# Optimization experiments

Hardware: AMD Instinct MI355X
Metric: run time of the kernel (lower is better)

Reference implementation:

```python
import jax, jax.numpy as jnp
import numpy as np

N, K, D = 50000, 32, 128


def setup_inputs() -> dict:
    key = jax.random.key(0)
    k1, k2, k3, k4 = jax.random.split(key, 4)
    v_fea = jax.random.normal(k1, (N, D), dtype=jnp.float32)
    t_emb = jax.random.normal(k2, (N, D), dtype=jnp.float32)
    ef = jax.random.randint(k3, (N, K), 0, N, dtype=jnp.int64)
    # nn.Linear(2D, 2D, bias=False) weight, scaled like torch default init
    W = jax.random.normal(k4, (2 * D, 2 * D), dtype=jnp.float32) * (1.0 / np.sqrt(2 * D))
    return {"v_fea": v_fea, "t_emb": t_emb, "ef": ef, "W": W}


def reference(v_fea, t_emb, ef, W):
    # v: gathered neighbor features [N, K, D]
    v = v_fea[ef]
    # q: [N, 2D]; torch Linear applies x @ W.T
    q = jnp.concatenate([v_fea, t_emb], axis=-1)
    wq = q @ W.T                                   # [N, 2D]
    # k: [N, K, 2D]
    k = jnp.concatenate([v, t_emb[ef]], axis=-1)
    # per-edge score: bmm(k, wq[..., None]) -> [N, K]
    r = jnp.einsum("nkd,nd->nk", k, wq)
    r = jax.nn.softmax(r, axis=1)                  # softmax over neighbors
    # weighted sum over neighbors -> [N, D]
    ef_fea = jnp.einsum("nk,nkd->nd", r, v)
    return ef_fea
```

## Files before the change

kernel.cpp:

```cpp
#include <hip/hip_runtime.h>
#include <hip/hip_bf16.h>

#define D     128
#define TWO_D 256
#define KNB   32

typedef __attribute__((ext_vector_type(8))) short    s8;
typedef __attribute__((ext_vector_type(8))) _Float16 h8;
typedef __attribute__((ext_vector_type(2))) _Float16 h2v;
typedef __attribute__((ext_vector_type(4))) float    f4;

__device__ inline unsigned short f2h(float f) {
    return __builtin_bit_cast(unsigned short, (_Float16)f);
}
__device__ inline float h2f(unsigned int u) {
    return (float)__builtin_bit_cast(_Float16, (unsigned short)u);
}

union v16u { s8 s; h2v h[4]; };

__device__ inline float dot8(s8 x, s8 w, float acc) {
#if __has_builtin(__builtin_amdgcn_fdot2)
    v16u ux, uw; ux.s = x; uw.s = w;
#pragma unroll
    for (int j = 0; j < 4; ++j)
        acc = __builtin_amdgcn_fdot2(ux.h[j], uw.h[j], acc, false);
#else
#pragma unroll
    for (int j = 0; j < 8; ++j)
        acc = fmaf(h2f((unsigned short)x[j]), h2f((unsigned short)w[j]), acc);
#endif
    return acc;
}

__device__ __forceinline__ void gload16(const void* g, void* l) {
    __builtin_amdgcn_global_load_lds(
        (__attribute__((address_space(1))) void*)g,
        (__attribute__((address_space(3))) void*)l, 16, 0, 0);
}

__global__ __launch_bounds__(256) void cast_kernel(
    const float* __restrict__ a, const float* __restrict__ b,
    unsigned short* __restrict__ oa, unsigned short* __restrict__ ob, int n4)
{
    int i = blockIdx.x * 256 + threadIdx.x;
    if (i >= n4) return;
    float4 x = ((const float4*)a)[i];
    float4 y = ((const float4*)b)[i];
    ushort4 px = make_ushort4(f2h(x.x), f2h(x.y), f2h(x.z), f2h(x.w));
    ushort4 py = make_ushort4(f2h(y.x), f2h(y.y), f2h(y.z), f2h(y.w));
    ((ushort4*)oa)[i] = px;
    ((ushort4*)ob)[i] = py;
}

#define BM 128
#define BN 64
#define BK 64
#define LDT 72

__global__ __launch_bounds__(256) void gemm_wq_mfma(
    const unsigned short* __restrict__ vh, const unsigned short* __restrict__ th,
    const float* __restrict__ W, unsigned short* __restrict__ wq_h, int M)
{
    __shared__ unsigned short As[BM][LDT];
    __shared__ unsigned short Bs[BN][LDT];

    const int tid  = threadIdx.x;
    const int w    = tid >> 6;
    const int lane = tid & 63;
    const int quad = lane >> 4;
    const int l16  = lane & 15;
    const int row0 = blockIdx.x * BM;
    const int i0   = blockIdx.y * BN;

    f4 acc[2][4] = {};

    const int arow = tid >> 1;
    const int acol = (tid & 1) * 32;
    int ga = row0 + arow; if (ga >= M) ga = M - 1;
    const int brow = tid >> 2;
    const int bcol = (tid & 3) * 16;

    for (int kt = 0; kt < TWO_D; kt += BK) {
        const unsigned short* srcA = (kt < D) ? vh : th;
        const int kb = kt & (D - 1);
        const unsigned short* pa = srcA + (size_t)ga * D + kb + acol;
        s8 a0 = *(const s8*)(pa);
        s8 a1 = *(const s8*)(pa + 8);
        s8 a2 = *(const s8*)(pa + 16);
        s8 a3 = *(const s8*)(pa + 24);
        const float* pb = W + (size_t)(i0 + brow) * TWO_D + kt + bcol;
        float4 b0 = *(const float4*)(pb);
        float4 b1 = *(const float4*)(pb + 4);
        float4 b2 = *(const float4*)(pb + 8);
        float4 b3 = *(const float4*)(pb + 12);

        __syncthreads();
        *(s8*)&As[arow][acol]      = a0;
        *(s8*)&As[arow][acol + 8]  = a1;
        *(s8*)&As[arow][acol + 16] = a2;
        *(s8*)&As[arow][acol + 24] = a3;
        {
            s8 q0, q1;
            q0[0]=(short)f2h(b0.x); q0[1]=(short)f2h(b0.y); q0[2]=(short)f2h(b0.z); q0[3]=(short)f2h(b0.w);
            q0[4]=(short)f2h(b1.x); q0[5]=(short)f2h(b1.y); q0[6]=(short)f2h(b1.z); q0[7]=(short)f2h(b1.w);
            q1[0]=(short)f2h(b2.x); q1[1]=(short)f2h(b2.y); q1[2]=(short)f2h(b2.z); q1[3]=(short)f2h(b2.w);
            q1[4]=(short)f2h(b3.x); q1[5]=(short)f2h(b3.y); q1[6]=(short)f2h(b3.z); q1[7]=(short)f2h(b3.w);
            *(s8*)&Bs[brow][bcol]     = q0;
            *(s8*)&Bs[brow][bcol + 8] = q1;
        }
        __syncthreads();

#pragma unroll
        for (int s = 0; s < 2; ++s) {
            s8 af0 = *(const s8*)&As[w * 32 + l16][s * 32 + quad * 8];
            s8 af1 = *(const s8*)&As[w * 32 + 16 + l16][s * 32 + quad * 8];
#pragma unroll
            for (int nt = 0; nt < 4; ++nt) {
                s8 bf = *(const s8*)&Bs[nt * 16 + l16][s * 32 + quad * 8];
                acc[0][nt] = __builtin_amdgcn_mfma_f32_16x16x32_f16(
                    __builtin_bit_cast(h8, af0), __builtin_bit_cast(h8, bf), acc[0][nt], 0, 0, 0);
                acc[1][nt] = __builtin_amdgcn_mfma_f32_16x16x32_f16(
                    __builtin_bit_cast(h8, af1), __builtin_bit_cast(h8, bf), acc[1][nt], 0, 0, 0);
            }
        }
    }

#pragma unroll
    for (int mt = 0; mt < 2; ++mt) {
#pragma unroll
        for (int nt = 0; nt < 4; ++nt) {
#pragma unroll
            for (int r = 0; r < 4; ++r) {
                int grow = row0 + w * 32 + mt * 16 + quad * 4 + r;
                if (grow < M)
                    wq_h[(size_t)grow * TWO_D + i0 + nt * 16 + l16] = f2h(acc[mt][nt][r]);
            }
        }
    }
}

__global__ __launch_bounds__(128) void attn_kernel(
    const unsigned short* __restrict__ vh, const unsigned short* __restrict__ th,
    const int* __restrict__ ef, const unsigned short* __restrict__ wq_h,
    float* __restrict__ outp, int M)
{
    __shared__ char L[2][17408];

    const int lane = threadIdx.x & 63;
    const int w    = threadIdx.x >> 6;
    const int n    = blockIdx.x * 2 + w;
    if (n >= M) return;

    char* Lw = &L[w][0];
    const int l16  = lane & 15;
    const int gsel = (lane >> 4) & 1;
    const unsigned short* gsrc = (lane < 32) ? vh : th;

    int eidx = 0;
    if (lane < KNB) eidx = ef[n * KNB + lane];

    gload16(wq_h + (size_t)n * TWO_D + lane * 8, Lw + 16384);
#pragma unroll
    for (int kk = 0; kk < 16; ++kk) {
        int e = __shfl(eidx, 2 * kk + gsel, 64);
        gload16(gsrc + (size_t)e * D + l16 * 8, Lw + kk * 1024);
    }
    __syncthreads();

    const int k     = lane & 31;
    const int tsel  = lane >> 5;
    const int dbase = (k >> 1) * 1024 + (k & 1) * 256 + tsel * 512;
    const int cbase = 16384 + tsel * 256;
    float p = 0.f;
#pragma unroll
    for (int j = 0; j < 16; ++j) {
        int jl = ((j + lane) & 15) * 16;
        s8 x = *(const s8*)(Lw + dbase + jl);
        s8 c = *(const s8*)(Lw + cbase + jl);
        p = dot8(x, c, p);
    }
    p += __shfl_xor(p, 32, 64);

    float mx = p;
#pragma unroll
    for (int off = 16; off > 0; off >>= 1) mx = fmaxf(mx, __shfl_xor(mx, off, 64));
    float ex  = __expf(p - mx);
    float sum = ex;
#pragma unroll
    for (int off = 16; off > 0; off >>= 1) sum += __shfl_xor(sum, off, 64);
    float r = ex / sum;

    float o4[4] = {0.f, 0.f, 0.f, 0.f};
    const int g   = lane >> 5;
    const int dby = (lane & 31) * 8;
#pragma unroll
    for (int kk = 0; kk < 16; ++kk) {
        float rk = __shfl(r, 2 * kk + g, 64);
        uint2 pq = *(const uint2*)(Lw + kk * 1024 + g * 256 + dby);
        o4[0] = fmaf(rk, h2f(pq.x & 0xFFFFu), o4[0]);
        o4[1] = fmaf(rk, h2f(pq.x >> 16),     o4[1]);
        o4[2] = fmaf(rk, h2f(pq.y & 0xFFFFu), o4[2]);
        o4[3] = fmaf(rk, h2f(pq.y >> 16),     o4[3]);
    }
#pragma unroll
    for (int j = 0; j < 4; ++j) o4[j] += __shfl_xor(o4[j], 32, 64);

    if (lane < 32)
        *(float4*)(outp + (size_t)n * D + (lane & 31) * 4) =
            make_float4(o4[0], o4[1], o4[2], o4[3]);
}

extern "C" void kernel_launch(void* const* d_in, const int* in_sizes, int n_in,
                              void* d_out, int out_size, void* d_ws, size_t ws_size,
                              hipStream_t stream)
{
    const float* v_fea = (const float*)d_in[0];
    const float* t_emb = (const float*)d_in[1];
    const int*   ef    = (const int*)d_in[2];
    const float* W     = (const float*)d_in[3];
    float* outp = (float*)d_out;

    const int M = in_sizes[0] / D;
    char* ws = (char*)d_ws;
    unsigned short* wq_h = (unsigned short*)ws;
    unsigned short* vh   = (unsigned short*)(ws + (size_t)M * TWO_D * 2);
    unsigned short* th   = (unsigned short*)(ws + (size_t)M * TWO_D * 2 + (size_t)M * D * 2);

    const int n4 = M * D / 4;
    cast_kernel<<<(n4 + 255) / 256, 256, 0, stream>>>(v_fea, t_emb, vh, th, n4);

    dim3 gg((M + BM - 1) / BM, TWO_D / BN);
    gemm_wq_mfma<<<gg, 256, 0, stream>>>(vh, th, W, wq_h, M);
    attn_kernel<<<M / 2, 128, 0, stream>>>(vh, th, ef, wq_h, outp, M);
}
```

Baseline: 238.6 us.

## Pre-cast W to fp16, single-shot swizzled GEMM tile, split attention rows across two waves

Result: slower. 243.6 us (+2.1%).

```diff
diff --git a/kernel.cpp b/kernel.cpp
--- a/kernel.cpp
+++ b/kernel.cpp
@@ -41,118 +41,100 @@
 
 __global__ __launch_bounds__(256) void cast_kernel(
     const float* __restrict__ a, const float* __restrict__ b,
-    unsigned short* __restrict__ oa, unsigned short* __restrict__ ob, int n4)
-{
-    int i = blockIdx.x * 256 + threadIdx.x;
-    if (i >= n4) return;
-    float4 x = ((const float4*)a)[i];
-    float4 y = ((const float4*)b)[i];
-    ushort4 px = make_ushort4(f2h(x.x), f2h(x.y), f2h(x.z), f2h(x.w));
-    ushort4 py = make_ushort4(f2h(y.x), f2h(y.y), f2h(y.z), f2h(y.w));
-    ((ushort4*)oa)[i] = px;
-    ((ushort4*)ob)[i] = py;
-}
-
-#define BM 128
-#define BN 64
-#define BK 64
-#define LDT 72
+    const float* __restrict__ Wsrc,
+    unsigned short* __restrict__ oa, unsigned short* __restrict__ ob,
+    unsigned short* __restrict__ oW, int n4, int nblkAB, int n4w)
+{
+    int bid = blockIdx.x;
+    if (bid < nblkAB) {
+        int i = bid * 256 + threadIdx.x;
+        if (i >= n4) return;
+        float4 x = ((const float4*)a)[i];
+        float4 y = ((const float4*)b)[i];
+        ((ushort4*)oa)[i] = make_ushort4(f2h(x.x), f2h(x.y), f2h(x.z), f2h(x.w));
+        ((ushort4*)ob)[i] = make_ushort4(f2h(y.x), f2h(y.y), f2h(y.z), f2h(y.w));
+    } else {
+        int i = (bid - nblkAB) * 256 + threadIdx.x;
+        if (i >= n4w) return;
+        float4 x = ((const float4*)Wsrc)[i];
+        ((ushort4*)oW)[i] = make_ushort4(f2h(x.x), f2h(x.y), f2h(x.z), f2h(x.w));
+    }
+}
 
 __global__ __launch_bounds__(256) void gemm_wq_mfma(
     const unsigned short* __restrict__ vh, const unsigned short* __restrict__ th,
-    const float* __restrict__ W, unsigned short* __restrict__ wq_h, int M)
-{
-    __shared__ unsigned short As[BM][LDT];
-    __shared__ unsigned short Bs[BN][LDT];
+    const unsigned short* __restrict__ Wh, unsigned short* __restrict__ wq_h, int M)
+{
+    __shared__ unsigned short Atile[64 * 256];
+    __shared__ unsigned short Btile[64 * 256];
 
     const int tid  = threadIdx.x;
-    const int w    = tid >> 6;
+    const int ww   = tid >> 6;
     const int lane = tid & 63;
     const int quad = lane >> 4;
     const int l16  = lane & 15;
-    const int row0 = blockIdx.x * BM;
-    const int i0   = blockIdx.y * BN;
-
-    f4 acc[2][4] = {};
-
-    const int arow = tid >> 1;
-    const int acol = (tid & 1) * 32;
-    int ga = row0 + arow; if (ga >= M) ga = M - 1;
-    const int brow = tid >> 2;
-    const int bcol = (tid & 3) * 16;
-
-    for (int kt = 0; kt < TWO_D; kt += BK) {
-        const unsigned short* srcA = (kt < D) ? vh : th;
-        const int kb = kt & (D - 1);
-        const unsigned short* pa = srcA + (size_t)ga * D + kb + acol;
-        s8 a0 = *(const s8*)(pa);
-        s8 a1 = *(const s8*)(pa + 8);
-        s8 a2 = *(const s8*)(pa + 16);
-        s8 a3 = *(const s8*)(pa + 24);
-        const float* pb = W + (size_t)(i0 + brow) * TWO_D + kt + bcol;
-        float4 b0 = *(const float4*)(pb);
-        float4 b1 = *(const float4*)(pb + 4);
-        float4 b2 = *(const float4*)(pb + 8);
-        float4 b3 = *(const float4*)(pb + 12);
-
-        __syncthreads();
-        *(s8*)&As[arow][acol]      = a0;
-        *(s8*)&As[arow][acol + 8]  = a1;
-        *(s8*)&As[arow][acol + 16] = a2;
-        *(s8*)&As[arow][acol + 24] = a3;
-        {
-            s8 q0, q1;
-            q0[0]=(short)f2h(b0.x); q0[1]=(short)f2h(b0.y); q0[2]=(short)f2h(b0.z); q0[3]=(short)f2h(b0.w);
-            q0[4]=(short)f2h(b1.x); q0[5]=(short)f2h(b1.y); q0[6]=(short)f2h(b1.z); q0[7]=(short)f2h(b1.w);
-            q1[0]=(short)f2h(b2.x); q1[1]=(short)f2h(b2.y); q1[2]=(short)f2h(b2.z); q1[3]=(short)f2h(b2.w);
-            q1[4]=(short)f2h(b3.x); q1[5]=(short)f2h(b3.y); q1[6]=(short)f2h(b3.z); q1[7]=(short)f2h(b3.w);
-            *(s8*)&Bs[brow][bcol]     = q0;
-            *(s8*)&Bs[brow][bcol + 8] = q1;
+    const int row0 = blockIdx.x * 64;
+    const int i0   = blockIdx.y * 64;
+
+    const int sr = tid >> 2, ss = tid & 3;
+    int ga = row0 + sr; if (ga >= M) ga = M - 1;
+    const unsigned short* asrc = ((ss < 2) ? vh : th) + (size_t)ga * D + (ss & 1) * 64;
+    const unsigned short* bsrc = Wh + (size_t)(i0 + sr) * TWO_D + ss * 64;
+
+    s8 av[8], bv[8];
+#pragma unroll
+    for (int m = 0; m < 8; ++m) av[m] = *(const s8*)(asrc + m * 8);
+#pragma unroll
+    for (int m = 0; m < 8; ++m) bv[m] = *(const s8*)(bsrc + m * 8);
+#pragma unroll
+    for (int m = 0; m < 8; ++m) {
+        int kblk = ss * 8 + m;
+        *(s8*)&Atile[sr * 256 + ((kblk ^ (sr & 7)) * 8)] = av[m];
+        *(s8*)&Btile[sr * 256 + ((kblk ^ (sr & 7)) * 8)] = bv[m];
+    }
+    __syncthreads();
+
+    f4 acc[4] = {};
+    const int ar = ww * 16 + l16;
+#pragma unroll
+    for (int s = 0; s < 8; ++s) {
+        int ablk = (s * 4 + quad) ^ (ar & 7);
+        s8 af = *(const s8*)&Atile[ar * 256 + ablk * 8];
+#pragma unroll
+        for (int nt = 0; nt < 4; ++nt) {
+            int br = nt * 16 + l16;
+            int bblk = (s * 4 + quad) ^ (br & 7);
+            s8 bf = *(const s8*)&Btile[br * 256 + bblk * 8];
+            acc[nt] = __builtin_amdgcn_mfma_f32_16x16x32_f16(
+                __builtin_bit_cast(h8, af), __builtin_bit_cast(h8, bf), acc[nt], 0, 0, 0);
         }
-        __syncthreads();
-
-#pragma unroll
-        for (int s = 0; s < 2; ++s) {
-            s8 af0 = *(const s8*)&As[w * 32 + l16][s * 32 + quad * 8];
-            s8 af1 = *(const s8*)&As[w * 32 + 16 + l16][s * 32 + quad * 8];
-#pragma unroll
-            for (int nt = 0; nt < 4; ++nt) {
-                s8 bf = *(const s8*)&Bs[nt * 16 + l16][s * 32 + quad * 8];
-                acc[0][nt] = __builtin_amdgcn_mfma_f32_16x16x32_f16(
-                    __builtin_bit_cast(h8, af0), __builtin_bit_cast(h8, bf), acc[0][nt], 0, 0, 0);
-                acc[1][nt] = __builtin_amdgcn_mfma_f32_16x16x32_f16(
-                    __builtin_bit_cast(h8, af1), __builtin_bit_cast(h8, bf), acc[1][nt], 0, 0, 0);
-            }
+    }
+
+#pragma unroll
+    for (int nt = 0; nt < 4; ++nt) {
+#pragma unroll
+        for (int r = 0; r < 4; ++r) {
+            int grow = row0 + ww * 16 + quad * 4 + r;
+            if (grow < M)
+                wq_h[(size_t)grow * TWO_D + i0 + nt * 16 + l16] = f2h(acc[nt][r]);
         }
     }
-
-#pragma unroll
-    for (int mt = 0; mt < 2; ++mt) {
-#pragma unroll
-        for (int nt = 0; nt < 4; ++nt) {
-#pragma unroll
-            for (int r = 0; r < 4; ++r) {
-                int grow = row0 + w * 32 + mt * 16 + quad * 4 + r;
-                if (grow < M)
-                    wq_h[(size_t)grow * TWO_D + i0 + nt * 16 + l16] = f2h(acc[mt][nt][r]);
-            }
-        }
-    }
-}
-
-__global__ __launch_bounds__(128) void attn_kernel(
+}
+
+__global__ __launch_bounds__(256) void attn_kernel(
     const unsigned short* __restrict__ vh, const unsigned short* __restrict__ th,
     const int* __restrict__ ef, const unsigned short* __restrict__ wq_h,
     float* __restrict__ outp, int M)
 {
-    __shared__ char L[2][17408];
+    __shared__ char L[2][18432];
 
     const int lane = threadIdx.x & 63;
-    const int w    = threadIdx.x >> 6;
-    const int n    = blockIdx.x * 2 + w;
-    if (n >= M) return;
-
-    char* Lw = &L[w][0];
+    const int wid  = threadIdx.x >> 6;
+    const int rib  = wid >> 1;
+    const int wsub = wid & 1;
+    const int n    = blockIdx.x * 2 + rib;
+
+    char* Lw = &L[rib][0];
     const int l16  = lane & 15;
     const int gsel = (lane >> 4) & 1;
     const unsigned short* gsrc = (lane < 32) ? vh : th;
@@ -160,32 +142,38 @@
     int eidx = 0;
     if (lane < KNB) eidx = ef[n * KNB + lane];
 
-    gload16(wq_h + (size_t)n * TWO_D + lane * 8, Lw + 16384);
-#pragma unroll
-    for (int kk = 0; kk < 16; ++kk) {
-        int e = __shfl(eidx, 2 * kk + gsel, 64);
+    if (wsub == 0)
+        gload16(wq_h + (size_t)n * TWO_D + lane * 8, Lw + 16384);
+#pragma unroll
+    for (int c = 0; c < 8; ++c) {
+        int kk = wsub * 8 + c;
+        int e  = __shfl(eidx, 2 * kk + gsel, 64);
         gload16(gsrc + (size_t)e * D + l16 * 8, Lw + kk * 1024);
     }
     __syncthreads();
 
     const int k     = lane & 31;
     const int tsel  = lane >> 5;
-    const int dbase = (k >> 1) * 1024 + (k & 1) * 256 + tsel * 512;
-    const int cbase = 16384 + tsel * 256;
+    const int dbase = (k >> 1) * 1024 + (k & 1) * 256 + tsel * 512 + wsub * 128;
+    const int cbase = 16384 + tsel * 256 + wsub * 128;
     float p = 0.f;
 #pragma unroll
-    for (int j = 0; j < 16; ++j) {
-        int jl = ((j + lane) & 15) * 16;
+    for (int j = 0; j < 8; ++j) {
+        int jl = ((j + lane) & 7) * 16;
         s8 x = *(const s8*)(Lw + dbase + jl);
         s8 c = *(const s8*)(Lw + cbase + jl);
         p = dot8(x, c, p);
     }
     p += __shfl_xor(p, 32, 64);
-
-    float mx = p;
+    if (lane < 32) *(float*)(Lw + 16896 + wsub * 128 + k * 4) = p;
+    __syncthreads();
+
+    float s = *(const float*)(Lw + 16896 + k * 4)
+            + *(const float*)(Lw + 16896 + 128 + k * 4);
+    float mx = s;
 #pragma unroll
     for (int off = 16; off > 0; off >>= 1) mx = fmaxf(mx, __shfl_xor(mx, off, 64));
-    float ex  = __expf(p - mx);
+    float ex  = __expf(s - mx);
     float sum = ex;
 #pragma unroll
     for (int off = 16; off > 0; off >>= 1) sum += __shfl_xor(sum, off, 64);
@@ -195,7 +183,8 @@
     const int g   = lane >> 5;
     const int dby = (lane & 31) * 8;
 #pragma unroll
-    for (int kk = 0; kk < 16; ++kk) {
+    for (int c = 0; c < 8; ++c) {
+        int kk = wsub * 8 + c;
         float rk = __shfl(r, 2 * kk + g, 64);
         uint2 pq = *(const uint2*)(Lw + kk * 1024 + g * 256 + dby);
         o4[0] = fmaf(rk, h2f(pq.x & 0xFFFFu), o4[0]);
@@ -205,10 +194,17 @@
     }
 #pragma unroll
     for (int j = 0; j < 4; ++j) o4[j] += __shfl_xor(o4[j], 32, 64);
-
     if (lane < 32)
-        *(float4*)(outp + (size_t)n * D + (lane & 31) * 4) =
+        *(float4*)(Lw + 17408 + wsub * 512 + lane * 16) =
             make_float4(o4[0], o4[1], o4[2], o4[3]);
+    __syncthreads();
+
+    if (wsub == 0 && lane < 32) {
+        float4 a = *(const float4*)(Lw + 17408 + lane * 16);
+        float4 b = *(const float4*)(Lw + 17408 + 512 + lane * 16);
+        *(float4*)(outp + (size_t)n * D + lane * 4) =
+            make_float4(a.x + b.x, a.y + b.y, a.z + b.z, a.w + b.w);
+    }
 }
 
 extern "C" void kernel_launch(void* const* d_in, const int* in_sizes, int n_in,
@@ -226,11 +222,16 @@
     unsigned short* wq_h = (unsigned short*)ws;
     unsigned short* vh   = (unsigned short*)(ws + (size_t)M * TWO_D * 2);
     unsigned short* th   = (unsigned short*)(ws + (size_t)M * TWO_D * 2 + (size_t)M * D * 2);
-
-    const int n4 = M * D / 4;
-    cast_kernel<<<(n4 + 255) / 256, 256, 0, stream>>>(v_fea, t_emb, vh, th, n4);
-
-    dim3 gg((M + BM - 1) / BM, TWO_D / BN);
-    gemm_wq_mfma<<<gg, 256, 0, stream>>>(vh, th, W, wq_h, M);
-    attn_kernel<<<M / 2, 128, 0, stream>>>(vh, th, ef, wq_h, outp, M);
-}
+    unsigned short* Wh   = (unsigned short*)(ws + (size_t)M * TWO_D * 2 + 2 * (size_t)M * D * 2);
+
+    const int n4     = M * D / 4;
+    const int nblkAB = (n4 + 255) / 256;
+    const int n4w    = TWO_D * TWO_D / 4;
+    const int nblkW  = (n4w + 255) / 256;
+    cast_kernel<<<nblkAB + nblkW, 256, 0, stream>>>(v_fea, t_emb, W, vh, th, Wh,
+                                                    n4, nblkAB, n4w);
+
+    dim3 gg((M + 63) / 64, 4);
+    gemm_wq_mfma<<<gg, 256, 0, stream>>>(vh, th, Wh, wq_h, M);
+    attn_kernel<<<M / 2, 256, 0, stream>>>(vh, th, ef, wq_h, outp, M);
+}
```
